# Kernel tuning notes

Hardware: AMD Instinct MI355X
Metric: run time of the kernel (lower is better)

## Reference

```python
import jax, jax.numpy as jnp
import numpy as np

D_MODEL = 2048
HQ = 32          # query heads
HKV = 8          # kv heads
HD = D_MODEL // HQ   # head_dim = 64
G = HQ // HKV        # group size = 4
THETA = 10000.0


def _rope(x, pos):
    """x: (B, H, T, D), pos: (B, T) int. Rotates even/odd interleaved pairs."""
    D = x.shape[-1]
    inv_freq = THETA ** (-jnp.arange(0, D, 2, dtype=jnp.float32) / D)   # (D/2,)
    ang = pos[:, None, :, None].astype(jnp.float32) * inv_freq          # (B,1,T,D/2)
    cos, sin = jnp.cos(ang), jnp.sin(ang)
    x1, x2 = x[..., 0::2], x[..., 1::2]
    r1 = x1 * cos - x2 * sin
    r2 = x1 * sin + x2 * cos
    return jnp.stack([r1, r2], axis=-1).reshape(x.shape)


def setup_inputs() -> dict:
    key = jax.random.key(0)
    ks = jax.random.split(key, 5)
    B, T = 2, 2048
    s = lambda fan_in: 1.0 / np.sqrt(fan_in)
    return {
        "x": jax.random.normal(ks[0], (B, T, D_MODEL), jnp.float32),
        "token_positions": jnp.arange(T, dtype=jnp.int32),
        "WQ": jax.random.normal(ks[1], (HQ * HD, D_MODEL), jnp.float32) * s(D_MODEL),
        "WK": jax.random.normal(ks[2], (HKV * HD, D_MODEL), jnp.float32) * s(D_MODEL),
        "WV": jax.random.normal(ks[3], (HKV * HD, D_MODEL), jnp.float32) * s(D_MODEL),
        "WO": jax.random.normal(ks[4], (D_MODEL, HQ * HD), jnp.float32) * s(HQ * HD),
    }


def reference(x, token_positions, WQ, WK, WV, WO):
    B, T, _ = x.shape
    pos = token_positions if token_positions.ndim == 2 else jnp.broadcast_to(token_positions[None, :], (B, T))

    # Projections (Linear is y = x @ W.T, no bias)
    Q = (x @ WQ.T).reshape(B, T, HQ, HD).transpose(0, 2, 1, 3)    # (B,Hq,T,D)
    K = (x @ WK.T).reshape(B, T, HKV, HD).transpose(0, 2, 1, 3)   # (B,Hkv,T,D)
    V = (x @ WV.T).reshape(B, T, HKV, HD).transpose(0, 2, 1, 3)

    Q = _rope(Q, pos)
    K = _rope(K, pos)

    # GQA: group query heads per kv head instead of duplicating K/V
    Qg = Q.reshape(B, HKV, G, T, HD)
    scale = jnp.float32(1.0 / np.sqrt(HD))
    scores = jnp.einsum('bkgqd,bkld->bkgql', Qg, K) * scale       # (B,Hkv,G,T,T)

    causal = jnp.tril(jnp.ones((T, T), dtype=bool))
    scores = jnp.where(causal, scores, jnp.finfo(scores.dtype).min)
    A = jax.nn.softmax(scores, axis=-1)

    O = jnp.einsum('bkgql,bkld->bkgqd', A, V)                     # (B,Hkv,G,T,D)
    O = O.reshape(B, HQ, T, HD).transpose(0, 2, 1, 3).reshape(B, T, HQ * HD)
    return O @ WO.T
```

## Files before the change

### kernel.cpp

```cpp
#include <hip/hip_runtime.h>
#include <hip/hip_bf16.h>

#define B_   2
#define T_   2048
#define DM_  2048
#define HQ_  32
#define HKV_ 8
#define HD_  64

typedef __attribute__((ext_vector_type(8))) short bf16x8;
typedef __attribute__((ext_vector_type(4))) float f32x4;
typedef __fp16 f16x4 __attribute__((ext_vector_type(4)));
typedef __fp16 f16x2 __attribute__((ext_vector_type(2)));

__device__ __forceinline__ unsigned short f2bf(float f) {
    unsigned int u = __float_as_uint(f);
    u = (u + 0x7fffu + ((u >> 16) & 1u)) >> 16;
    return (unsigned short)u;
}

__device__ __forceinline__ void gload16(const unsigned short* g, unsigned short* l) {
    __builtin_amdgcn_global_load_lds(
        (const __attribute__((address_space(1))) unsigned int*)g,
        (__attribute__((address_space(3))) unsigned int*)l, 16, 0, 0);
}


__global__ __launch_bounds__(256) void convert_all(
    const float* __restrict__ x,  const float* __restrict__ WQ,
    const float* __restrict__ WK, const float* __restrict__ WV,
    const float* __restrict__ WO, unsigned short* __restrict__ ws)
{
    int i = blockIdx.x*256 + threadIdx.x;
    const float* src; unsigned short* dst; int rel;
    if (i < 2097152)      { src = x;  dst = ws;                 rel = i; }
    else if (i < 3145728) { src = WQ; dst = ws + 8388608;       rel = i - 2097152; }
    else if (i < 3407872) { src = WK; dst = ws + 8388608+4194304; rel = i - 3145728; }
    else if (i < 3670016) { src = WV; dst = ws + 8388608+5242880; rel = i - 3407872; }
    else                  { src = WO; dst = ws + 14680064;      rel = i - 3670016; }
    float4 v = *(const float4*)(src + (size_t)rel*4);
    uint2 pk;
    pk.x = (unsigned int)f2bf(v.x) | ((unsigned int)f2bf(v.y) << 16);
    pk.y = (unsigned int)f2bf(v.z) | ((unsigned int)f2bf(v.w) << 16);
    *(uint2*)(dst + (size_t)rel*4) = pk;
}

__global__ __launch_bounds__(256) void qkv_gemm_bf16(
    const unsigned short* __restrict__ Ab, const unsigned short* __restrict__ Wb,
    unsigned short* __restrict__ Qb, unsigned short* __restrict__ Kb,
    unsigned short* __restrict__ Vt)
{
    __shared__ unsigned short As[2][128*32];
    __shared__ unsigned short Bs[2][128*32];
    const int tid  = threadIdx.x;
    const int ln   = tid & 63;
    const int wv   = tid >> 6;
    const int wm   = (wv >> 1) * 64;
    const int wn   = (wv & 1) * 64;
    const int col  = ln & 15;
    const int quad = ln >> 4;
    const int m0   = blockIdx.y * 128;
    const int n0   = blockIdx.x * 128;

    const int cg = ((tid & 3) ^ ((tid >> 3) & 3)) * 8;
    const unsigned short* aG = Ab + (size_t)(m0 + (tid>>2))*DM_ + cg;
    const unsigned short* bG = Wb + (size_t)(n0 + (tid>>2))*DM_ + cg;
    const int ck = (quad ^ ((col >> 1) & 3)) * 8;

    f32x4 acc[4][4];
    #pragma unroll
    for (int i=0;i<4;++i)
        #pragma unroll
        for (int j=0;j<4;++j) { acc[i][j][0]=0.f; acc[i][j][1]=0.f; acc[i][j][2]=0.f; acc[i][j][3]=0.f; }

    {
        unsigned short* aL = &As[0][wv*512];
        unsigned short* bL = &Bs[0][wv*512];
        gload16(aG,                  aL);
        gload16(aG + (size_t)64*DM_, aL + 2048);
        gload16(bG,                  bL);
        gload16(bG + (size_t)64*DM_, bL + 2048);
    }
    __syncthreads();

    int cur = 0;
    for (int k0 = 0; k0 < DM_; k0 += 32) {
        if (k0 + 32 < DM_) {
            unsigned short* aL = &As[cur^1][wv*512];
            unsigned short* bL = &Bs[cur^1][wv*512];
            gload16(aG + k0 + 32,                  aL);
            gload16(aG + (size_t)64*DM_ + k0 + 32, aL + 2048);
            gload16(bG + k0 + 32,                  bL);
            gload16(bG + (size_t)64*DM_ + k0 + 32, bL + 2048);
        }
        bf16x8 af[4], bfr[4];
        #pragma unroll
        for (int i=0;i<4;++i) {
            af[i]  = *(const bf16x8*)&As[cur][(wm + i*16 + col)*32 + ck];
            bfr[i] = *(const bf16x8*)&Bs[cur][(wn + i*16 + col)*32 + ck];
        }
        #pragma unroll
        for (int i=0;i<4;++i)
            #pragma unroll
            for (int j=0;j<4;++j)
                acc[i][j] = __builtin_amdgcn_mfma_f32_16x16x32_bf16(af[i], bfr[j], acc[i][j], 0, 0, 0);
        __syncthreads();
        cur ^= 1;
    }

    const int b  = m0 >> 11;
    const int tb = m0 & 2047;
    #pragma unroll
    for (int j=0;j<4;++j) {
        const int n = n0 + wn + j*16 + col;
        #pragma unroll
        for (int i=0;i<4;++i) {
            const int t = tb + wm + i*16 + quad*4;
            if (n < 2048) {
                #pragma unroll
                for (int r=0;r<4;++r)
                    Qb[(((size_t)(b*HQ_ + (n>>6)))*T_ + t + r)*HD_ + (n&63)] = f2bf(acc[i][j][r]);
            } else if (n < 2560) {
                #pragma unroll
                for (int r=0;r<4;++r)
                    Kb[(((size_t)(b*HKV_ + ((n-2048)>>6)))*T_ + t + r)*HD_ + (n&63)] = f2bf(acc[i][j][r]);
            } else {
                unsigned short* vp = Vt + (((size_t)(b*HKV_ + ((n-2560)>>6)))*HD_ + (n&63))*T_ + t;
                union { f16x2 h; unsigned int u; } c0, c1;
                c0.h = __builtin_amdgcn_cvt_pkrtz(acc[i][j][0], acc[i][j][1]);
                c1.h = __builtin_amdgcn_cvt_pkrtz(acc[i][j][2], acc[i][j][3]);
                *(unsigned int*)(vp)     = c0.u;
                *(unsigned int*)(vp + 2) = c1.u;
            }
        }
    }
}

__global__ __launch_bounds__(256) void rope_inplace(
    unsigned short* __restrict__ Qb, unsigned short* __restrict__ Kb,
    const int* __restrict__ pos)
{
    const int NQ = B_*HQ_*T_*(HD_/2);
    const int NK = B_*HKV_*T_*(HD_/2);
    int idx = blockIdx.x*256 + threadIdx.x;
    unsigned short* base; float scale;
    int rem;
    if (idx < NQ) { base = Qb; rem = idx; scale = 0.18033688011112042f; }
    else { rem = idx - NQ; if (rem >= NK) return; base = Kb; scale = 1.0f; }
    const int i  = rem & 31;
    const int t  = (rem >> 5) & (T_ - 1);
    const int bh = rem >> 16;
    size_t off = (((size_t)bh)*T_ + t)*HD_ + (i<<1);
    unsigned int pk = *(unsigned int*)(base + off);
    float x1 = __uint_as_float((pk & 0xffffu) << 16);
    float x2 = __uint_as_float(pk & 0xffff0000u);
    float p = (float)pos[t];
    float inv = exp2f(-13.287712379549449f * ((float)(i<<1)) * (1.0f/64.0f));
    float ang = p * inv;
    float sn, cs;
    sincosf(ang, &sn, &cs);
    float r1 = (x1*cs - x2*sn) * scale;
    float r2 = (x1*sn + x2*cs) * scale;
    unsigned int out = (unsigned int)f2bf(r1) | ((unsigned int)f2bf(r2) << 16);
    *(unsigned int*)(base + off) = out;
}

__global__ __launch_bounds__(256, 2) void attn_mfma(
    const unsigned short* __restrict__ Qb, const unsigned short* __restrict__ Kb,
    const unsigned short* __restrict__ Vh, unsigned short* __restrict__ Ob)
{
    __shared__ unsigned short Ks[2][64*64];
    __shared__ unsigned short Vs[2][64*64];

    const int tid  = threadIdx.x;
    const int lane = tid & 63;
    const int wave = tid >> 6;
    const int q16  = lane & 15;
    const int quad = lane >> 4;
    const int bxi  = blockIdx.x;
    const int bh   = blockIdx.y;
    const int b    = bh >> 5;
    const int h    = bh & 31;
    const int kvh  = h >> 2;
    const int qa   = bxi;
    const int qbt  = 31 - bxi;
    const int qgA  = qa *64 + wave*16 + q16;
    const int qgB  = qbt*64 + wave*16 + q16;

    const unsigned short* kbase = Kb + ((size_t)(b*HKV_ + kvh))*T_*HD_;
    const unsigned short* vbase = Vh + ((size_t)(b*HKV_ + kvh))*(size_t)HD_*T_;

    const bf16x8 qA0 = *(const bf16x8*)(Qb + ((size_t)bh*T_ + qgA)*HD_ + quad*8);
    const bf16x8 qA1 = *(const bf16x8*)(Qb + ((size_t)bh*T_ + qgA)*HD_ + 32 + quad*8);
    const bf16x8 qB0 = *(const bf16x8*)(Qb + ((size_t)bh*T_ + qgB)*HD_ + quad*8);
    const bf16x8 qB1 = *(const bf16x8*)(Qb + ((size_t)bh*T_ + qgB)*HD_ + 32 + quad*8);

    f32x4 oA[4], oB[4];
    #pragma unroll
    for (int i=0;i<4;++i) {
        oA[i][0]=0.f; oA[i][1]=0.f; oA[i][2]=0.f; oA[i][3]=0.f;
        oB[i][0]=0.f; oB[i][1]=0.f; oB[i][2]=0.f; oB[i][3]=0.f;
    }
    float lA = 0.f, lB = 0.f;

    const int sr = tid >> 3;
    const int sj = tid & 7;
    const int sc = (sj ^ (sr & 7)) * 8;

    const int rk7 = q16 & 7;
    const int ck0 = (quad ^ rk7) * 8;
    const int ck1 = ((quad + 4) ^ rk7) * 8;

    auto smrow = [&](const f32x4 s, float& ps) -> f16x4 {
        float e0 = exp2f(s[0]), e1 = exp2f(s[1]);
        float e2 = exp2f(s[2]), e3 = exp2f(s[3]);
        ps += (e0+e1) + (e2+e3);
        union { f16x2 h[2]; f16x4 v; } c;
        c.h[0] = __builtin_amdgcn_cvt_pkrtz(e0, e1);
        c.h[1] = __builtin_amdgcn_cvt_pkrtz(e2, e3);
        return c.v;
    };

    uint4 kr0, kr1, vr0, vr1;
    kr0 = *(const uint4*)(kbase + (size_t)sr*HD_ + sj*8);
    kr1 = *(const uint4*)(kbase + (size_t)(sr+32)*HD_ + sj*8);
    vr0 = *(const uint4*)(vbase + (size_t)sr*T_ + sj*8);
    vr1 = *(const uint4*)(vbase + (size_t)(sr+32)*T_ + sj*8);
    *(uint4*)&Ks[0][sr*64 + sc]      = kr0;
    *(uint4*)&Ks[0][(sr+32)*64 + sc] = kr1;
    *(uint4*)&Vs[0][sr*64 + sc]      = vr0;
    *(uint4*)&Vs[0][(sr+32)*64 + sc] = vr1;
    kr0 = *(const uint4*)(kbase + (size_t)(64+sr)*HD_ + sj*8);
    kr1 = *(const uint4*)(kbase + (size_t)(64+sr+32)*HD_ + sj*8);
    vr0 = *(const uint4*)(vbase + (size_t)sr*T_ + 64 + sj*8);
    vr1 = *(const uint4*)(vbase + (size_t)(sr+32)*T_ + 64 + sj*8);
    __syncthreads();

    int cur = 0;

    for (int kt = 0; kt <= qa; ++kt) {
        const unsigned short* KsC = Ks[cur];
        const unsigned short* VsC = Vs[cur];
        const int nxt = cur ^ 1;

        f32x4 sB[4], sA[4];
        #pragma unroll
        for (int t=0;t<4;++t) {
            sB[t][0]=0.f; sB[t][1]=0.f; sB[t][2]=0.f; sB[t][3]=0.f;
            sA[t][0]=0.f; sA[t][1]=0.f; sA[t][2]=0.f; sA[t][3]=0.f;
        }
        f16x4 pfB[4];
        float psB = 0.f, psA = 0.f;

        __builtin_amdgcn_s_setprio(1);
        #pragma unroll
        for (int t = 0; t < 4; ++t) {
            const int rk = (t*16 + q16) * 64;
            bf16x8 a0 = *(const bf16x8*)&KsC[rk + ck0];
            bf16x8 a1 = *(const bf16x8*)&KsC[rk + ck1];
            sB[t] = __builtin_amdgcn_mfma_f32_16x16x32_bf16(a0, qB0, sB[t], 0, 0, 0);
            sB[t] = __builtin_amdgcn_mfma_f32_16x16x32_bf16(a1, qB1, sB[t], 0, 0, 0);
            sA[t] = __builtin_amdgcn_mfma_f32_16x16x32_bf16(a0, qA0, sA[t], 0, 0, 0);
            sA[t] = __builtin_amdgcn_mfma_f32_16x16x32_bf16(a1, qA1, sA[t], 0, 0, 0);
            if (t > 0) pfB[t-1] = smrow(sB[t-1], psB);
        }
        *(uint4*)&Ks[nxt][sr*64 + sc]      = kr0;
        *(uint4*)&Ks[nxt][(sr+32)*64 + sc] = kr1;
        *(uint4*)&Vs[nxt][sr*64 + sc]      = vr0;
        *(uint4*)&Vs[nxt][(sr+32)*64 + sc] = vr1;
        if (kt + 1 < qbt) {
            const int kn = (kt+2)*64;
            kr0 = *(const uint4*)(kbase + (size_t)(kn+sr)*HD_ + sj*8);
            kr1 = *(const uint4*)(kbase + (size_t)(kn+sr+32)*HD_ + sj*8);
            vr0 = *(const uint4*)(vbase + (size_t)sr*T_ + kn + sj*8);
            vr1 = *(const uint4*)(vbase + (size_t)(sr+32)*T_ + kn + sj*8);
        }
        pfB[3] = smrow(sB[3], psB);
        lB += psB;

        if (kt == qa) {
            #pragma unroll
            for (int t = 0; t < 4; ++t)
                #pragma unroll
                for (int r = 0; r < 4; ++r)
                    if (kt*64 + t*16 + quad*4 + r > qgA) sA[t][r] = -1e30f;
        }

        #pragma unroll
        for (int t = 0; t < 4; ++t) {
            const int cv = ((2*t + (quad>>1)) ^ rk7) * 8 + (quad&1)*4;
            f16x4 va[4];
            #pragma unroll
            for (int dt=0;dt<4;++dt)
                va[dt] = *(const f16x4*)&VsC[(dt*16 + q16)*64 + cv];
            #pragma unroll
            for (int dt=0;dt<4;++dt)
                oB[dt] = __builtin_amdgcn_mfma_f32_16x16x16f16(va[dt], pfB[t], oB[dt], 0, 0, 0);
            f16x4 pfA = smrow(sA[t], psA);
            #pragma unroll
            for (int dt=0;dt<4;++dt)
                oA[dt] = __builtin_amdgcn_mfma_f32_16x16x16f16(va[dt], pfA, oA[dt], 0, 0, 0);
        }
        lA += psA;
        __builtin_amdgcn_s_setprio(0);
        __syncthreads();
        cur ^= 1;
    }

    for (int kt = qa+1; kt <= qbt; ++kt) {
        const unsigned short* KsC = Ks[cur];
        const unsigned short* VsC = Vs[cur];
        const int nxt = cur ^ 1;

        f32x4 sB[4];
        #pragma unroll
        for (int t=0;t<4;++t) { sB[t][0]=0.f; sB[t][1]=0.f; sB[t][2]=0.f; sB[t][3]=0.f; }

        __builtin_amdgcn_s_setprio(1);
        #pragma unroll
        for (int t = 0; t < 4; ++t) {
            const int rk = (t*16 + q16) * 64;
            bf16x8 a0 = *(const bf16x8*)&KsC[rk + ck0];
            bf16x8 a1 = *(const bf16x8*)&KsC[rk + ck1];
            sB[t] = __builtin_amdgcn_mfma_f32_16x16x32_bf16(a0, qB0, sB[t], 0, 0, 0);
            sB[t] = __builtin_amdgcn_mfma_f32_16x16x32_bf16(a1, qB1, sB[t], 0, 0, 0);
        }
        if (kt < qbt) {
            *(uint4*)&Ks[nxt][sr*64 + sc]      = kr0;
            *(uint4*)&Ks[nxt][(sr+32)*64 + sc] = kr1;
            *(uint4*)&Vs[nxt][sr*64 + sc]      = vr0;
            *(uint4*)&Vs[nxt][(sr+32)*64 + sc] = vr1;
        }
        if (kt + 1 < qbt) {
            const int kn = (kt+2)*64;
            kr0 = *(const uint4*)(kbase + (size_t)(kn+sr)*HD_ + sj*8);
            kr1 = *(const uint4*)(kbase + (size_t)(kn+sr+32)*HD_ + sj*8);
            vr0 = *(const uint4*)(vbase + (size_t)sr*T_ + kn + sj*8);
            vr1 = *(const uint4*)(vbase + (size_t)(sr+32)*T_ + kn + sj*8);
        }
        if (kt == qbt) {
            #pragma unroll
            for (int t = 0; t < 4; ++t)
                #pragma unroll
                for (int r = 0; r < 4; ++r)
                    if (kt*64 + t*16 + quad*4 + r > qgB) sB[t][r] = -1e30f;
        }

        float psB = 0.f;
        #pragma unroll
        for (int t = 0; t < 4; ++t) {
            f16x4 pfB = smrow(sB[t], psB);
            const int cv = ((2*t + (quad>>1)) ^ rk7) * 8 + (quad&1)*4;
            #pragma unroll
            for (int dt=0;dt<4;++dt) {
                f16x4 va = *(const f16x4*)&VsC[(dt*16 + q16)*64 + cv];
                oB[dt] = __builtin_amdgcn_mfma_f32_16x16x16f16(va, pfB, oB[dt], 0, 0, 0);
            }
        }
        lB += psB;
        __builtin_amdgcn_s_setprio(0);
        __syncthreads();
        cur ^= 1;
    }

    lA += __shfl_xor(lA, 16); lA += __shfl_xor(lA, 32);
    lB += __shfl_xor(lB, 16); lB += __shfl_xor(lB, 32);
    const float rlA = 1.0f / lA;
    const float rlB = 1.0f / lB;
    unsigned short* opA = Ob + ((size_t)(b*T_ + qgA))*(HQ_*HD_) + h*HD_;
    unsigned short* opB = Ob + ((size_t)(b*T_ + qgB))*(HQ_*HD_) + h*HD_;
    #pragma unroll
    for (int dt = 0; dt < 4; ++dt) {
        uint2 pa, pb;
        pa.x = (unsigned int)f2bf(oA[dt][0]*rlA) | ((unsigned int)f2bf(oA[dt][1]*rlA) << 16);
        pa.y = (unsigned int)f2bf(oA[dt][2]*rlA) | ((unsigned int)f2bf(oA[dt][3]*rlA) << 16);
        pb.x = (unsigned int)f2bf(oB[dt][0]*rlB) | ((unsigned int)f2bf(oB[dt][1]*rlB) << 16);
        pb.y = (unsigned int)f2bf(oB[dt][2]*rlB) | ((unsigned int)f2bf(oB[dt][3]*rlB) << 16);
        *(uint2*)(opA + dt*16 + quad*4) = pa;
        *(uint2*)(opB + dt*16 + quad*4) = pb;
    }
}

__global__ __launch_bounds__(256) void out_gemm_bf16(
    const unsigned short* __restrict__ Ab, const unsigned short* __restrict__ Wb,
    float* __restrict__ C)
{
    __shared__ unsigned short As[2][128*32];
    __shared__ unsigned short Bs[2][128*32];
    const int tid  = threadIdx.x;
    const int ln   = tid & 63;
    const int wv   = tid >> 6;
    const int wm   = (wv >> 1) * 64;
    const int wn   = (wv & 1) * 64;
    const int col  = ln & 15;
    const int quad = ln >> 4;
    const int m0   = blockIdx.y * 128;
    const int n0   = blockIdx.x * 128;

    const int cg = ((tid & 3) ^ ((tid >> 3) & 3)) * 8;
    const unsigned short* aG = Ab + (size_t)(m0 + (tid>>2))*DM_ + cg;
    const unsigned short* bG = Wb + (size_t)(n0 + (tid>>2))*DM_ + cg;
    const int ck = (quad ^ ((col >> 1) & 3)) * 8;

    f32x4 acc[4][4];
    #pragma unroll
    for (int i=0;i<4;++i)
        #pragma unroll
        for (int j=0;j<4;++j) { acc[i][j][0]=0.f; acc[i][j][1]=0.f; acc[i][j][2]=0.f; acc[i][j][3]=0.f; }

    {
        unsigned short* aL = &As[0][wv*512];
        unsigned short* bL = &Bs[0][wv*512];
        gload16(aG,                  aL);
        gload16(aG + (size_t)64*DM_, aL + 2048);
        gload16(bG,                  bL);
        gload16(bG + (size_t)64*DM_, bL + 2048);
    }
    __syncthreads();

    int cur = 0;
    for (int k0 = 0; k0 < DM_; k0 += 32) {
        if (k0 + 32 < DM_) {
            unsigned short* aL = &As[cur^1][wv*512];
            unsigned short* bL = &Bs[cur^1][wv*512];
            gload16(aG + k0 + 32,                  aL);
            gload16(aG + (size_t)64*DM_ + k0 + 32, aL + 2048);
            gload16(bG + k0 + 32,                  bL);
            gload16(bG + (size_t)64*DM_ + k0 + 32, bL + 2048);
        }
        bf16x8 af[4], bfr[4];
        #pragma unroll
        for (int i=0;i<4;++i) {
            af[i]  = *(const bf16x8*)&As[cur][(wm + i*16 + col)*32 + ck];
            bfr[i] = *(const bf16x8*)&Bs[cur][(wn + i*16 + col)*32 + ck];
        }
        #pragma unroll
        for (int i=0;i<4;++i)
            #pragma unroll
            for (int j=0;j<4;++j)
                acc[i][j] = __builtin_amdgcn_mfma_f32_16x16x32_bf16(af[i], bfr[j], acc[i][j], 0, 0, 0);
        __syncthreads();
        cur ^= 1;
    }

    #pragma unroll
    for (int i=0;i<4;++i) {
        const int m = m0 + wm + i*16 + quad*4;
        #pragma unroll
        for (int j=0;j<4;++j) {
            const int n = n0 + wn + j*16 + col;
            #pragma unroll
            for (int r=0;r<4;++r)
                C[(size_t)(m + r)*DM_ + n] = acc[i][j][r];
        }
    }
}

extern "C" void kernel_launch(void* const* d_in, const int* in_sizes, int n_in,
                              void* d_out, int out_size, void* d_ws, size_t ws_size,
                              hipStream_t stream) {
    const float* x   = (const float*)d_in[0];
    const int*   pos = (const int*)  d_in[1];
    const float* WQ  = (const float*)d_in[2];
    const float* WK  = (const float*)d_in[3];
    const float* WV  = (const float*)d_in[4];
    const float* WO  = (const float*)d_in[5];
    float* out = (float*)d_out;

    unsigned short* xb  = (unsigned short*)d_ws;
    unsigned short* Wb  = xb  + (size_t)8388608;
    unsigned short* WOb = Wb  + (size_t)6291456;
    unsigned short* Qb  = WOb + (size_t)4194304;
    unsigned short* Kb  = Qb  + (size_t)8388608;
    unsigned short* Vt  = Kb  + (size_t)2097152;
    unsigned short* Ob  = Vt  + (size_t)2097152;

    convert_all<<<18432, 256, 0, stream>>>(x, WQ, WK, WV, WO, (unsigned short*)d_ws);

    dim3 g1(24, 32);
    qkv_gemm_bf16<<<g1, 256, 0, stream>>>(xb, Wb, Qb, Kb, Vt);

    const int pairs = B_*HQ_*T_*(HD_/2) + B_*HKV_*T_*(HD_/2);
    rope_inplace<<<(pairs + 255)/256, 256, 0, stream>>>(Qb, Kb, pos);

    dim3 g3(16, B_*HQ_);
    attn_mfma<<<g3, 256, 0, stream>>>(Qb, Kb, Vt, Ob);

    dim3 g4(16, 32);
    out_gemm_bf16<<<g4, 256, 0, stream>>>(Ob, WOb, out);
}
```

Measured before the change: 335.3 us.

## Triple-buffer GEMM LDS pipeline and swizzle block order for XCD locality

Both projection GEMMs move from a double-buffered LDS loop to a three-stage buffer. Loads are issued two k-tiles ahead, with explicit vmcnt waits and a single barrier per iteration, so global-to-LDS latency overlaps with the MFMA work. The grids become 1D and block IDs are remapped so consecutive blocks on the same XCD (bid&7) cover neighbouring tiles, aiming at better L2 reuse. The cost is 50% more LDS per block, which may lower occupancy, plus reliance on hand-set vmcnt counts for correctness.

```diff
diff --git a/kernel.cpp b/kernel.cpp
--- a/kernel.cpp
+++ b/kernel.cpp
@@ -50,8 +50,8 @@
     unsigned short* __restrict__ Qb, unsigned short* __restrict__ Kb,
     unsigned short* __restrict__ Vt)
 {
-    __shared__ unsigned short As[2][128*32];
-    __shared__ unsigned short Bs[2][128*32];
+    __shared__ unsigned short As[3][128*32];
+    __shared__ unsigned short Bs[3][128*32];
     const int tid  = threadIdx.x;
     const int ln   = tid & 63;
     const int wv   = tid >> 6;
@@ -59,8 +59,11 @@
     const int wn   = (wv & 1) * 64;
     const int col  = ln & 15;
     const int quad = ln >> 4;
-    const int m0   = blockIdx.y * 128;
-    const int n0   = blockIdx.x * 128;
+
+    const int bid = blockIdx.x;
+    const int swz = (bid & 7) * 96 + (bid >> 3);
+    const int n0  = (swz % 24) * 128;
+    const int m0  = (swz / 24) * 128;
 
     const int cg = ((tid & 3) ^ ((tid >> 3) & 3)) * 8;
     const unsigned short* aG = Ab + (size_t)(m0 + (tid>>2))*DM_ + cg;
@@ -73,39 +76,40 @@
         #pragma unroll
         for (int j=0;j<4;++j) { acc[i][j][0]=0.f; acc[i][j][1]=0.f; acc[i][j][2]=0.f; acc[i][j][3]=0.f; }
 
-    {
-        unsigned short* aL = &As[0][wv*512];
-        unsigned short* bL = &Bs[0][wv*512];
-        gload16(aG,                  aL);
-        gload16(aG + (size_t)64*DM_, aL + 2048);
-        gload16(bG,                  bL);
-        gload16(bG + (size_t)64*DM_, bL + 2048);
-    }
-    __syncthreads();
-
-    int cur = 0;
-    for (int k0 = 0; k0 < DM_; k0 += 32) {
+    auto stage = [&](int buf, int k0) {
+        unsigned short* aL = &As[buf][wv*512];
+        unsigned short* bL = &Bs[buf][wv*512];
+        gload16(aG + k0,                  aL);
+        gload16(aG + (size_t)64*DM_ + k0, aL + 2048);
+        gload16(bG + k0,                  bL);
+        gload16(bG + (size_t)64*DM_ + k0, bL + 2048);
+    };
+
+    stage(0, 0);
+    stage(1, 32);
+
+    int kt = 0;
+    for (int k0 = 0; k0 < DM_; k0 += 32, ++kt) {
         if (k0 + 32 < DM_) {
-            unsigned short* aL = &As[cur^1][wv*512];
-            unsigned short* bL = &Bs[cur^1][wv*512];
-            gload16(aG + k0 + 32,                  aL);
-            gload16(aG + (size_t)64*DM_ + k0 + 32, aL + 2048);
-            gload16(bG + k0 + 32,                  bL);
-            gload16(bG + (size_t)64*DM_ + k0 + 32, bL + 2048);
-        }
+            asm volatile("s_waitcnt vmcnt(4)" ::: "memory");
+        } else {
+            asm volatile("s_waitcnt vmcnt(0)" ::: "memory");
+        }
+        __builtin_amdgcn_s_barrier();
+        if (k0 + 64 < DM_) stage((kt+2)%3, k0 + 64);
+        const unsigned short* Ac = As[kt%3];
+        const unsigned short* Bc = Bs[kt%3];
         bf16x8 af[4], bfr[4];
         #pragma unroll
         for (int i=0;i<4;++i) {
-            af[i]  = *(const bf16x8*)&As[cur][(wm + i*16 + col)*32 + ck];
-            bfr[i] = *(const bf16x8*)&Bs[cur][(wn + i*16 + col)*32 + ck];
+            af[i]  = *(const bf16x8*)&Ac[(wm + i*16 + col)*32 + ck];
+            bfr[i] = *(const bf16x8*)&Bc[(wn + i*16 + col)*32 + ck];
         }
         #pragma unroll
         for (int i=0;i<4;++i)
             #pragma unroll
             for (int j=0;j<4;++j)
                 acc[i][j] = __builtin_amdgcn_mfma_f32_16x16x32_bf16(af[i], bfr[j], acc[i][j], 0, 0, 0);
-        __syncthreads();
-        cur ^= 1;
     }
 
     const int b  = m0 >> 11;
@@ -385,8 +389,8 @@
     const unsigned short* __restrict__ Ab, const unsigned short* __restrict__ Wb,
     float* __restrict__ C)
 {
-    __shared__ unsigned short As[2][128*32];
-    __shared__ unsigned short Bs[2][128*32];
+    __shared__ unsigned short As[3][128*32];
+    __shared__ unsigned short Bs[3][128*32];
     const int tid  = threadIdx.x;
     const int ln   = tid & 63;
     const int wv   = tid >> 6;
@@ -394,8 +398,11 @@
     const int wn   = (wv & 1) * 64;
     const int col  = ln & 15;
     const int quad = ln >> 4;
-    const int m0   = blockIdx.y * 128;
-    const int n0   = blockIdx.x * 128;
+
+    const int bid = blockIdx.x;
+    const int swz = (bid & 7) * 64 + (bid >> 3);
+    const int n0  = (swz & 15) * 128;
+    const int m0  = (swz >> 4) * 128;
 
     const int cg = ((tid & 3) ^ ((tid >> 3) & 3)) * 8;
     const unsigned short* aG = Ab + (size_t)(m0 + (tid>>2))*DM_ + cg;
@@ -408,39 +415,40 @@
         #pragma unroll
         for (int j=0;j<4;++j) { acc[i][j][0]=0.f; acc[i][j][1]=0.f; acc[i][j][2]=0.f; acc[i][j][3]=0.f; }
 
-    {
-        unsigned short* aL = &As[0][wv*512];
-        unsigned short* bL = &Bs[0][wv*512];
-        gload16(aG,                  aL);
-        gload16(aG + (size_t)64*DM_, aL + 2048);
-        gload16(bG,                  bL);
-        gload16(bG + (size_t)64*DM_, bL + 2048);
-    }
-    __syncthreads();
-
-    int cur = 0;
-    for (int k0 = 0; k0 < DM_; k0 += 32) {
+    auto stage = [&](int buf, int k0) {
+        unsigned short* aL = &As[buf][wv*512];
+        unsigned short* bL = &Bs[buf][wv*512];
+        gload16(aG + k0,                  aL);
+        gload16(aG + (size_t)64*DM_ + k0, aL + 2048);
+        gload16(bG + k0,                  bL);
+        gload16(bG + (size_t)64*DM_ + k0, bL + 2048);
+    };
+
+    stage(0, 0);
+    stage(1, 32);
+
+    int kt = 0;
+    for (int k0 = 0; k0 < DM_; k0 += 32, ++kt) {
         if (k0 + 32 < DM_) {
-            unsigned short* aL = &As[cur^1][wv*512];
-            unsigned short* bL = &Bs[cur^1][wv*512];
-            gload16(aG + k0 + 32,                  aL);
-            gload16(aG + (size_t)64*DM_ + k0 + 32, aL + 2048);
-            gload16(bG + k0 + 32,                  bL);
-            gload16(bG + (size_t)64*DM_ + k0 + 32, bL + 2048);
-        }
+            asm volatile("s_waitcnt vmcnt(4)" ::: "memory");
+        } else {
+            asm volatile("s_waitcnt vmcnt(0)" ::: "memory");
+        }
+        __builtin_amdgcn_s_barrier();
+        if (k0 + 64 < DM_) stage((kt+2)%3, k0 + 64);
+        const unsigned short* Ac = As[kt%3];
+        const unsigned short* Bc = Bs[kt%3];
         bf16x8 af[4], bfr[4];
         #pragma unroll
         for (int i=0;i<4;++i) {
-            af[i]  = *(const bf16x8*)&As[cur][(wm + i*16 + col)*32 + ck];
-            bfr[i] = *(const bf16x8*)&Bs[cur][(wn + i*16 + col)*32 + ck];
+            af[i]  = *(const bf16x8*)&Ac[(wm + i*16 + col)*32 + ck];
+            bfr[i] = *(const bf16x8*)&Bc[(wn + i*16 + col)*32 + ck];
         }
         #pragma unroll
         for (int i=0;i<4;++i)
             #pragma unroll
             for (int j=0;j<4;++j)
                 acc[i][j] = __builtin_amdgcn_mfma_f32_16x16x32_bf16(af[i], bfr[j], acc[i][j], 0, 0, 0);
-        __syncthreads();
-        cur ^= 1;
     }
 
     #pragma unroll
@@ -477,8 +485,7 @@
 
     convert_all<<<18432, 256, 0, stream>>>(x, WQ, WK, WV, WO, (unsigned short*)d_ws);
 
-    dim3 g1(24, 32);
-    qkv_gemm_bf16<<<g1, 256, 0, stream>>>(xb, Wb, Qb, Kb, Vt);
+    qkv_gemm_bf16<<<768, 256, 0, stream>>>(xb, Wb, Qb, Kb, Vt);
 
     const int pairs = B_*HQ_*T_*(HD_/2) + B_*HKV_*T_*(HD_/2);
     rope_inplace<<<(pairs + 255)/256, 256, 0, stream>>>(Qb, Kb, pos);
@@ -486,6 +493,5 @@
     dim3 g3(16, B_*HQ_);
     attn_mfma<<<g3, 256, 0, stream>>>(Qb, Kb, Vt, Ob);
 
-    dim3 g4(16, 32);
-    out_gemm_bf16<<<g4, 256, 0, stream>>>(Ob, WOb, out);
-}
+    out_gemm_bf16<<<512, 256, 0, stream>>>(Ob, WOb, out);
+}
```

Measured after the change: 333.1 us. No clear change (-0.7%).
